# Kernel tuning notes

Measured on AMD Instinct MI355X. Metric: run time of the kernel, lower is better.

The kernel has to match this reference:

```python
import jax, jax.numpy as jnp
import numpy as np

B, S, D, L = 8, 512, 768, 200


def leaky(x, slope=0.2):
    return jnp.where(x >= 0, x, slope * x)


def l1_normalize(x, axis):
    # torch.nn.functional.normalize(p=1): x / max(sum|x|, 1e-12)
    return x / jnp.maximum(jnp.sum(jnp.abs(x), axis=axis, keepdims=True), 1e-12)


def setup_inputs() -> dict:
    key = jax.random.key(0)
    ks = jax.random.split(key, 16)
    s = 1.0 / np.sqrt(D)
    return {
        "doc_embedding": jax.random.normal(ks[0], (B, S, D), jnp.float32),
        "labels": jax.random.uniform(ks[1], (B, L), jnp.float32),
        "label_embed": jax.random.normal(ks[2], (L, D), jnp.float32),
        "label_adj": jax.random.uniform(ks[3], (L, L), jnp.float32),
        "w_gcn3": jax.random.uniform(ks[4], (D, D), jnp.float32, -s, s),
        "w_gcn5": jax.random.uniform(ks[5], (D, D), jnp.float32, -s, s),
        "w_ll1": jax.random.normal(ks[6], (D, D), jnp.float32) * s,
        "b_ll1": jax.random.normal(ks[7], (D,), jnp.float32) * s,
        "w_ll2": jax.random.normal(ks[8], (D, D), jnp.float32) * s,
        "b_ll2": jax.random.normal(ks[9], (D,), jnp.float32) * s,
        "w_lin": jax.random.normal(ks[10], (2 * D, D), jnp.float32) * (1.0 / np.sqrt(2 * D)),
        "b_lin": jax.random.normal(ks[11], (D,), jnp.float32) * s,
        "conv_w": jax.random.normal(ks[12], (L, 1, 9, 9), jnp.float32) * (1.0 / 9.0),
        "conv_b": jax.random.normal(ks[13], (L,), jnp.float32) * 0.01,
        "w_lin1": jax.random.normal(ks[14], (D, L), jnp.float32) * s,
        "b_lin1": jax.random.normal(ks[15], (L,), jnp.float32) * s,
    }


def reference(doc_embedding, labels, label_embed, label_adj, w_gcn3, w_gcn5,
              w_ll1, b_ll1, w_ll2, b_ll2, w_lin, b_lin, conv_w, conv_b,
              w_lin1, b_lin1):
    b = doc_embedding.shape[0]
    # stacked (replicated) label embeddings: [B, L, D]
    le = jnp.broadcast_to(label_embed, (b,) + label_embed.shape)

    # GCN3: adj @ (x @ W), leaky relu 0.2
    le = leaky(jnp.einsum('lm,bmd->bld', label_adj, le @ w_gcn3))

    # learned adjacency A = sigmoid(lin1(le) @ lin2(le)^T)   [B, L, L]
    q = le @ w_ll1 + b_ll1
    k = le @ w_ll2 + b_ll2
    A = jax.nn.sigmoid(jnp.einsum('bld,bmd->blm', q, k))

    # normalize_adj: D^{-1/2} with detached row sum; out = (A D)^T D
    row_sum = jax.lax.stop_gradient(jnp.sum(A, axis=1))  # [B, L]
    d_inv_sqrt = jnp.where(row_sum > 0, row_sum ** -0.5, 0.0)
    AD = A * d_inv_sqrt[:, None, :]                 # A @ diag(d)
    A_norm = jnp.swapaxes(AD, 1, 2) * d_inv_sqrt[:, None, :]

    # GCN5 with learned adj
    d_le = leaky(jnp.einsum('blm,bmd->bld', A_norm, le @ w_gcn5))

    le_cat = jnp.concatenate([le, d_le], axis=-1)   # [B, L, 2D]
    le_out = le_cat @ w_lin + b_lin                 # [B, L, D]

    le_out = l1_normalize(le_out, axis=-2)
    doc = l1_normalize(doc_embedding, axis=-2)

    # word-label attention map [B, S, L]
    wla = jnp.einsum('bsd,bld->bsl', doc, le_out)

    # conv2d 1 -> L channels, 9x9, pad 4 over [B, 1, S, L]
    att = jax.lax.conv_general_dilated(
        wla[:, None, :, :], conv_w, window_strides=(1, 1),
        padding=((4, 4), (4, 4)),
        dimension_numbers=('NCHW', 'OIHW', 'NCHW'))
    att = att + conv_b[None, :, None, None]         # [B, L, S, L]

    att = jnp.max(att, axis=1)                      # [B, S, L]
    att = jnp.max(att, axis=-1, keepdims=True)      # [B, S, 1]
    gate = jnp.tanh(att)

    h_enc = jnp.sum(gate * doc, axis=1)             # [B, D]
    label_output = jax.nn.sigmoid(h_enc @ w_lin1 + b_lin1)

    eps = 1e-7
    p = jnp.clip(label_output, eps, 1.0 - eps)
    loss = -jnp.mean(labels * jnp.log(p) + (1.0 - labels) * jnp.log(1.0 - p))
    return label_output, loss
```

## Files before the change

### kernel.cpp

```cpp
#include <hip/hip_runtime.h>
#include <hip/hip_bf16.h>
#include <math.h>

#define BB 8
#define SS 512
#define DD 768
#define LL 200

typedef __attribute__((ext_vector_type(8))) short bf16x8;
typedef __attribute__((ext_vector_type(4))) float f32x4;

__device__ inline short f2bf(float f) {
    unsigned u = __builtin_bit_cast(unsigned, f);
    unsigned r = (u + 0x7FFFu + ((u >> 16) & 1u)) >> 16;
    return (short)r;
}

#define LDP2 72

template<int EPI, bool TB>
__global__ __launch_bounds__(256) void mgemm_k(
    const short* __restrict__ A, int lda,
    const void* __restrict__ Bv, int ldb,
    const float* __restrict__ bias,
    const void* __restrict__ Bv2, const float* __restrict__ bias2, int nsplit,
    const void* __restrict__ Bv3, const float* __restrict__ bias3, int nsplit2,
    float* __restrict__ Cf, int ldc,
    short* __restrict__ Cb, int ldcb,
    short* __restrict__ Ct, int ldct, int nsplitT,
    int M, int N, int K)
{
    __shared__ __align__(16) short As[64 * LDP2];
    __shared__ __align__(16) short Bs[64 * LDP2];
    const int tid = threadIdx.x;
    const int bm = blockIdx.y * 64;
    const int bn = blockIdx.x * 64;
    int bnb = bn;
    if (!TB) {
        if (bn >= nsplit2)      { Bv = Bv3; bias = bias3; bnb = bn - nsplit2; }
        else if (bn >= nsplit)  { Bv = Bv2; bias = bias2; bnb = bn - nsplit; }
    }
    const int w = tid >> 6, lane = tid & 63, g = lane >> 4, ln = lane & 15;
    const int Kp = (K + 63) & ~63;
    const int nt = Kp >> 6;

    const int ar = tid >> 2, ac = tid & 3;
    const int bkk = tid >> 2, bc = tid & 3;

    f32x4 acc[4];
    #pragma unroll
    for (int i = 0; i < 4; ++i) acc[i] = (f32x4){0.f, 0.f, 0.f, 0.f};

    bf16x8 aR0 = {0,0,0,0,0,0,0,0}, aR1 = {0,0,0,0,0,0,0,0};
    bf16x8 bR0 = {0,0,0,0,0,0,0,0}, bR1 = {0,0,0,0,0,0,0,0};
    float  bF[16];
    #pragma unroll
    for (int j = 0; j < 16; ++j) bF[j] = 0.f;

    const int gmS = bm + ar;
    const bool aOk = (gmS < M);

    auto fetchA = [&](int k0) {
        if (aOk) {
            const short* p = A + (size_t)gmS * lda + k0 + ac * 16;
            aR0 = *(const bf16x8*)p;
            aR1 = *(const bf16x8*)(p + 8);
        }
    };
    auto fetchB = [&](int k0) {
        if (TB) {
            const short* Bt = (const short*)Bv;
            int gn = bn + ar;
            if (gn < N) {
                const short* p = Bt + (size_t)gn * ldb + k0 + ac * 16;
                bR0 = *(const bf16x8*)p;
                bR1 = *(const bf16x8*)(p + 8);
            }
        } else {
            const float* Bp = (const float*)Bv;
            int gk = k0 + bkk;
            int n0 = bnb + bc * 16;
            int gn0 = bn + bc * 16;
            if (gk < K) {
                const float* p = Bp + (size_t)gk * ldb + n0;
                if (gn0 + 16 <= N) {
                    #pragma unroll
                    for (int q = 0; q < 4; ++q) {
                        float4 x = *(const float4*)(p + q * 4);
                        bF[q*4+0]=x.x; bF[q*4+1]=x.y; bF[q*4+2]=x.z; bF[q*4+3]=x.w;
                    }
                } else {
                    #pragma unroll
                    for (int j = 0; j < 16; ++j) bF[j] = (gn0 + j < N) ? p[j] : 0.f;
                }
            } else {
                #pragma unroll
                for (int j = 0; j < 16; ++j) bF[j] = 0.f;
            }
        }
    };

    fetchA(0);
    fetchB(0);

    for (int t = 0; t < nt; ++t) {
        {
            short* pa = As + ar * LDP2 + ac * 16;
            *(bf16x8*)pa = aR0;
            *(bf16x8*)(pa + 8) = aR1;
        }
        if (TB) {
            short* pb = Bs + ar * LDP2 + ac * 16;
            *(bf16x8*)pb = bR0;
            *(bf16x8*)(pb + 8) = bR1;
        } else {
            #pragma unroll
            for (int j = 0; j < 16; ++j)
                Bs[(bc * 16 + j) * LDP2 + bkk] = f2bf(bF[j]);
        }
        __syncthreads();

        if (t + 1 < nt) {
            int k0 = (t + 1) << 6;
            fetchA(k0);
            fetchB(k0);
        }

        #pragma unroll
        for (int ks = 0; ks < 2; ++ks) {
            bf16x8 a = *(const bf16x8*)(As + (w * 16 + ln) * LDP2 + ks * 32 + g * 8);
            #pragma unroll
            for (int nb = 0; nb < 4; ++nb) {
                bf16x8 b = *(const bf16x8*)(Bs + (nb * 16 + ln) * LDP2 + ks * 32 + g * 8);
                acc[nb] = __builtin_amdgcn_mfma_f32_16x16x32_bf16(a, b, acc[nb], 0, 0, 0);
            }
        }
        __syncthreads();
    }

    #pragma unroll
    for (int nb = 0; nb < 4; ++nb) {
        int gn = bn + nb * 16 + ln;
        float bv = (bias && gn < N) ? bias[bnb + nb * 16 + ln] : 0.f;
        #pragma unroll
        for (int r = 0; r < 4; ++r) {
            int gm = bm + w * 16 + g * 4 + r;
            if (gm < M && gn < N) {
                float v = acc[nb][r] + bv;
                if (EPI == 1) v = (v >= 0.f) ? v : 0.2f * v;
                else if (EPI == 2) v = 1.f / (1.f + expf(-v));
                if (Cf) Cf[(size_t)gm * ldc + gn] = v;
                if (Cb) Cb[(size_t)gm * ldcb + gn] = f2bf(v);
                if (Ct && gn >= nsplitT)
                    Ct[(size_t)(gn - nsplitT) * ldct + gm] = f2bf(v);
            }
        }
    }
}

#define WP 168
#define TP 24
#define WTR 217
#define WROWS 208
#define APAD 256
#define BIGN (1 << 30)

__global__ void prep_k(const float* __restrict__ cw, const float* __restrict__ cb,
                       const float* __restrict__ adj,
                       short* __restrict__ wkg, short* __restrict__ adj_bf)
{
    int idx = blockIdx.x * blockDim.x + threadIdx.x;
    if (idx < WROWS * WP) {
        int o = idx / WP, kk = idx % WP;
        int kj = kk >> 4, ki = kk & 15;
        float v = 0.f;
        if (o < LL && kj < 9) {
            if (ki < 9) v = cw[o * 81 + ki * 9 + kj];
            else if (ki == 9 && kj == 0) v = cb[o];
        }
        wkg[idx] = f2bf(v);
        return;
    }
    idx -= WROWS * WP;
    if (idx < LL * APAD) {
        int r = idx / APAD, c = idx % APAD;
        adj_bf[idx] = f2bf(c < LL ? adj[r * LL + c] : 0.f);
    }
}

__global__ void ca_k(const float* __restrict__ A, short* __restrict__ An)
{
    int i = blockIdx.x;
    int j = threadIdx.x;
    float si = 0.f, sj = 0.f;
    for (int l = 0; l < LL; ++l) {
        si += A[l * LL + i];
        if (j < LL) sj += A[l * LL + j];
    }
    float di = (si > 0.f) ? (1.f / sqrtf(si)) : 0.f;
    float dj = (sj > 0.f) ? (1.f / sqrtf(sj)) : 0.f;
    float v = (j < LL) ? A[j * LL + i] * di * dj : 0.f;
    An[i * APAD + j] = f2bf(v);
}

__global__ void l1n_k(const float* __restrict__ X, short* __restrict__ Xb)
{
    int c = threadIdx.x >> 5, r = threadIdx.x & 31;
    int col = blockIdx.x * 8 + c;
    float s = 0.f;
    for (int l = r; l < LL; l += 32) s += fabsf(X[l * DD + col]);
    #pragma unroll
    for (int off = 16; off > 0; off >>= 1) s += __shfl_xor(s, off, 64);
    float inv = 1.f / fmaxf(s, 1e-12f);
    for (int l = r; l < LL; l += 32)
        Xb[l * DD + col] = f2bf(X[l * DD + col] * inv);
}

__global__ void docsum_k(const float* __restrict__ doc, float* __restrict__ denom)
{
    int dc = blockIdx.x, b = blockIdx.y;
    int dx = threadIdx.x & 63, sy = threadIdx.x >> 6;
    int d = dc * 64 + dx;
    float s = 0.f;
    for (int t = sy; t < SS; t += 4)
        s += fabsf(doc[((size_t)b * SS + t) * DD + d]);
    __shared__ float red[4][64];
    red[sy][dx] = s;
    __syncthreads();
    if (sy == 0)
        denom[b * DD + d] = fmaxf(red[0][dx] + red[1][dx] + red[2][dx] + red[3][dx], 1e-12f);
}

__global__ void docbf_k(const float* __restrict__ doc, const float* __restrict__ denom,
                        short* __restrict__ docb)
{
    int gid = blockIdx.x * blockDim.x + threadIdx.x;
    if (gid >= BB * SS * DD / 4) return;
    size_t base = (size_t)gid * 4;
    int d = (int)(base % DD);
    int b = (int)(base / ((size_t)SS * DD));
    float4 v = *(const float4*)(doc + base);
    float4 dn = *(const float4*)(denom + b * DD + d);
    short4 o;
    o.x = f2bf(v.x / dn.x);
    o.y = f2bf(v.y / dn.y);
    o.z = f2bf(v.z / dn.z);
    o.w = f2bf(v.w / dn.w);
    *(short4*)(docb + base) = o;
}

__global__ __launch_bounds__(512, 1) void conv_max_k(
    const float* __restrict__ wla,
    const short* __restrict__ wkg,
    float* __restrict__ gate)
{
    extern __shared__ short smem[];
    short* Wk   = smem;
    short* winT = Wk + WROWS * WP;
    short* wbf  = winT + 4 * WTR * TP;
    __shared__ float wredf[8];

    const int blk = blockIdx.x;
    const int b = blk >> 7;
    const int s0 = (blk & 127) << 2;
    const int tid = threadIdx.x;

    {
        const int4* src = (const int4*)wkg;
        int4* dst = (int4*)Wk;
        for (int i = tid; i < WROWS * WP / 8; i += 512) dst[i] = src[i];
    }
    for (int idx = tid; idx < 12 * 216; idx += 512) {
        int r = idx / 216, c = idx % 216;
        int sr = s0 - 4 + r, col = c - 4;
        float v = 0.f;
        if (sr >= 0 && sr < SS && col >= 0 && col < LL)
            v = wla[((size_t)b * SS + sr) * LL + col];
        wbf[idx] = f2bf(v);
    }
    __syncthreads();
    for (int idx = tid; idx < 4 * WTR; idx += 512) {
        int p = idx / WTR, r = idx % WTR;
        short vals[16];
        #pragma unroll
        for (int i = 0; i < 9; ++i) vals[i] = (r < 216) ? wbf[(p + i) * 216 + r] : (short)0;
        vals[9] = (short)0x3F80;
        #pragma unroll
        for (int i = 10; i < 16; ++i) vals[i] = 0;
        short* dstp = winT + (p * WTR + r) * TP;
        *(bf16x8*)dstp = *(const bf16x8*)vals;
        *(bf16x8*)(dstp + 8) = *(const bf16x8*)(vals + 8);
    }
    __syncthreads();

    const int w = tid >> 6;
    const int p = w >> 1;
    const int h = w & 1;
    const int lane = tid & 63;
    const int g = lane >> 4;
    const int ln = lane & 15;
    const short* WT = winT + p * WTR * TP;

    bf16x8 Af[7][5];
    #pragma unroll
    for (int s = 0; s < 7; ++s) {
        int st = h * 7 + s;
        if (st > 12) st = 12;
        #pragma unroll
        for (int j = 0; j < 5; ++j)
            Af[s][j] = *(const bf16x8*)(Wk + (st * 16 + ln) * WP + j * 32 + g * 8);
    }

    float lm = -INFINITY;

    auto loadB = [&](int nt, bf16x8 (&Bf)[5]) {
        #pragma unroll
        for (int j = 0; j < 5; ++j)
            Bf[j] = *(const bf16x8*)(WT + (nt * 16 + ln + 2 * j + (g >> 1)) * TP + (g & 1) * 8);
    };
    auto compute = [&](int nt, const bf16x8 (&Bf)[5]) {
        #pragma unroll
        for (int s = 0; s < 7; ++s) {
            if (h == 0 || s < 6) {
                int st = h * 7 + s;
                f32x4 acc = {0.f, 0.f, 0.f, 0.f};
                #pragma unroll
                for (int j = 0; j < 5; ++j)
                    acc = __builtin_amdgcn_mfma_f32_16x16x32_bf16(Af[s][j], Bf[j], acc, 0, 0, 0);
                float t = fmaxf(fmaxf(acc[0], acc[1]), fmaxf(acc[2], acc[3]));
                bool ok = (st < 12 || g < 2) && (nt < 12 || ln < 8);
                lm = ok ? fmaxf(lm, t) : lm;
            }
        }
    };

    bf16x8 B0[5], B1[5];
    loadB(0, B0);
    for (int nt = 0; nt < 12; nt += 2) {
        loadB(nt + 1, B1);
        compute(nt, B0);
        loadB(nt + 2, B0);
        compute(nt + 1, B1);
    }
    compute(12, B0);

    #pragma unroll
    for (int off = 32; off > 0; off >>= 1)
        lm = fmaxf(lm, __shfl_xor(lm, off, 64));
    if (lane == 0) wredf[w] = lm;
    __syncthreads();
    if (tid < 4)
        gate[((size_t)b << 9) + s0 + tid] = tanhf(fmaxf(wredf[2 * tid], wredf[2 * tid + 1]));
}

__global__ void henc_part_k(const float* __restrict__ doc, const float* __restrict__ gate,
                            float* __restrict__ hpart)
{
    int dc = blockIdx.x, sc = blockIdx.y, b = blockIdx.z;
    int dx = threadIdx.x & 63, sy = threadIdx.x >> 6;
    int d = dc * 64 + dx;
    float s = 0.f;
    for (int t = sy; t < 64; t += 4) {
        int srow = sc * 64 + t;
        s = fmaf(doc[((size_t)b * SS + srow) * DD + d], gate[b * SS + srow], s);
    }
    __shared__ float red[4][64];
    red[sy][dx] = s;
    __syncthreads();
    if (sy == 0)
        hpart[((size_t)b * 8 + sc) * DD + d] = red[0][dx] + red[1][dx] + red[2][dx] + red[3][dx];
}

__global__ void final2_k(const float* __restrict__ hpart, const float* __restrict__ denom,
                         const float* __restrict__ W, const float* __restrict__ bias,
                         float* __restrict__ out)
{
    int b = blockIdx.x, tid = threadIdx.x;
    __shared__ float hb[DD];
    for (int idx = tid; idx < DD; idx += 256) {
        float s = 0.f;
        #pragma unroll
        for (int sc = 0; sc < 8; ++sc) s += hpart[((size_t)b * 8 + sc) * DD + idx];
        hb[idx] = s / denom[b * DD + idx];
    }
    __syncthreads();
    int l = tid;
    if (l < LL) {
        float acc = bias[l];
        for (int d = 0; d < DD; ++d) acc = fmaf(hb[d], W[d * LL + l], acc);
        out[b * LL + l] = 1.f / (1.f + expf(-acc));
    }
}

__global__ void loss_k(const float* __restrict__ out, const float* __restrict__ labels,
                       float* __restrict__ loss_out)
{
    float s = 0.f;
    for (int i = threadIdx.x; i < BB * LL; i += 256) {
        float p = out[i];
        p = fminf(fmaxf(p, 1e-7f), 1.f - 1e-7f);
        float y = labels[i];
        s += y * logf(p) + (1.f - y) * logf(1.f - p);
    }
    #pragma unroll
    for (int off = 32; off > 0; off >>= 1) s += __shfl_down(s, off, 64);
    __shared__ float ws[4];
    if ((threadIdx.x & 63) == 0) ws[threadIdx.x >> 6] = s;
    __syncthreads();
    if (threadIdx.x == 0)
        loss_out[0] = -(ws[0] + ws[1] + ws[2] + ws[3]) / (float)(BB * LL);
}

static void mgemm(hipStream_t st, int epi, bool tb,
                  const short* A, int lda, const void* B, int ldb,
                  const float* bias,
                  const void* B2, const float* bias2, int nsplit,
                  const void* B3, const float* bias3, int nsplit2,
                  float* Cf, int ldc, short* Cb, int ldcb,
                  short* Ct, int ldct, int nsplitT,
                  int M, int N, int K)
{
    dim3 g((N + 63) / 64, (M + 63) / 64);
    if (!tb) {
        if (epi == 0)      mgemm_k<0, false><<<g, 256, 0, st>>>(A, lda, B, ldb, bias, B2, bias2, nsplit, B3, bias3, nsplit2, Cf, ldc, Cb, ldcb, Ct, ldct, nsplitT, M, N, K);
        else if (epi == 1) mgemm_k<1, false><<<g, 256, 0, st>>>(A, lda, B, ldb, bias, B2, bias2, nsplit, B3, bias3, nsplit2, Cf, ldc, Cb, ldcb, Ct, ldct, nsplitT, M, N, K);
        else               mgemm_k<2, false><<<g, 256, 0, st>>>(A, lda, B, ldb, bias, B2, bias2, nsplit, B3, bias3, nsplit2, Cf, ldc, Cb, ldcb, Ct, ldct, nsplitT, M, N, K);
    } else {
        if (epi == 0)      mgemm_k<0, true><<<g, 256, 0, st>>>(A, lda, B, ldb, bias, B2, bias2, nsplit, B3, bias3, nsplit2, Cf, ldc, Cb, ldcb, Ct, ldct, nsplitT, M, N, K);
        else if (epi == 1) mgemm_k<1, true><<<g, 256, 0, st>>>(A, lda, B, ldb, bias, B2, bias2, nsplit, B3, bias3, nsplit2, Cf, ldc, Cb, ldcb, Ct, ldct, nsplitT, M, N, K);
        else               mgemm_k<2, true><<<g, 256, 0, st>>>(A, lda, B, ldb, bias, B2, bias2, nsplit, B3, bias3, nsplit2, Cf, ldc, Cb, ldcb, Ct, ldct, nsplitT, M, N, K);
    }
}

extern "C" void kernel_launch(void* const* d_in, const int* in_sizes, int n_in,
                              void* d_out, int out_size, void* d_ws, size_t ws_size,
                              hipStream_t stream)
{
    const float* doc_emb   = (const float*)d_in[0];
    const float* labels    = (const float*)d_in[1];
    const float* label_emb = (const float*)d_in[2];
    const float* label_adj = (const float*)d_in[3];
    const float* w_gcn3    = (const float*)d_in[4];
    const float* w_gcn5    = (const float*)d_in[5];
    const float* w_ll1     = (const float*)d_in[6];
    const float* b_ll1     = (const float*)d_in[7];
    const float* w_ll2     = (const float*)d_in[8];
    const float* b_ll2     = (const float*)d_in[9];
    const float* w_lin     = (const float*)d_in[10];
    const float* b_lin     = (const float*)d_in[11];
    const float* conv_w    = (const float*)d_in[12];
    const float* conv_b    = (const float*)d_in[13];
    const float* w_lin1    = (const float*)d_in[14];
    const float* b_lin1    = (const float*)d_in[15];

    float* out = (float*)d_out;

    char* p = (char*)d_ws;
    auto alloc = [&](size_t bytes) { void* r = p; p += (bytes + 15) & ~(size_t)15; return r; };
    short* wkg       = (short*)alloc(WROWS * WP * 2);
    short* adj_bf    = (short*)alloc(200 * APAD * 2);
    short* E2_bf     = (short*)alloc(200 * 768 * 2);
    short* le_cat_bf = (short*)alloc(200 * 1536 * 2);
    short* qkh_bf    = (short*)alloc(200 * 2304 * 2);
    short* Ht        = (short*)alloc(768 * 256 * 2);
    float* Amat      = (float*)alloc(200 * 200 * 4);
    short* Anorm_bf  = (short*)alloc(200 * APAD * 2);
    float* le_out_f  = (float*)alloc(200 * 768 * 4);
    short* le_out_bf = (short*)alloc(200 * 768 * 2);
    float* denom     = (float*)alloc(BB * DD * 4);
    short* doc_nb    = (short*)alloc((size_t)BB * SS * DD * 2);
    float* wla       = (float*)alloc((size_t)BB * SS * LL * 4);
    float* gatev     = (float*)alloc(BB * SS * 4);
    float* hpart     = (float*)alloc(BB * 8 * DD * 4);

    prep_k<<<(WROWS * WP + LL * APAD + 255) / 256, 256, 0, stream>>>(
        conv_w, conv_b, label_adj, wkg, adj_bf);
    mgemm(stream, 0, false, adj_bf, APAD, label_emb, DD, nullptr,
          nullptr, nullptr, BIGN, nullptr, nullptr, BIGN,
          nullptr, 0, E2_bf, DD, nullptr, 0, BIGN, LL, DD, LL);
    mgemm(stream, 1, false, E2_bf, DD, w_gcn3, DD, nullptr,
          nullptr, nullptr, BIGN, nullptr, nullptr, BIGN,
          nullptr, 0, le_cat_bf, 1536, nullptr, 0, BIGN, LL, DD, DD);
    mgemm(stream, 0, false, le_cat_bf, 1536, w_ll1, DD, b_ll1,
          w_ll2, b_ll2, DD, w_gcn5, nullptr, 2 * DD,
          nullptr, 0, qkh_bf, 2304, Ht, 256, 2 * DD, LL, 3 * DD, DD);
    mgemm(stream, 2, true, qkh_bf, 2304, qkh_bf + DD, 2304, nullptr,
          nullptr, nullptr, BIGN, nullptr, nullptr, BIGN,
          Amat, LL, nullptr, 0, nullptr, 0, BIGN, LL, LL, DD);
    ca_k<<<LL, 256, 0, stream>>>(Amat, Anorm_bf);
    mgemm(stream, 1, true, Anorm_bf, APAD, Ht, 256, nullptr,
          nullptr, nullptr, BIGN, nullptr, nullptr, BIGN,
          nullptr, 0, le_cat_bf + DD, 1536, nullptr, 0, BIGN, LL, DD, LL);
    mgemm(stream, 0, false, le_cat_bf, 1536, w_lin, DD, b_lin,
          nullptr, nullptr, BIGN, nullptr, nullptr, BIGN,
          le_out_f, DD, nullptr, 0, nullptr, 0, BIGN, LL, DD, 2 * DD);
    l1n_k<<<96, 256, 0, stream>>>(le_out_f, le_out_bf);
    docsum_k<<<dim3(12, 8), 256, 0, stream>>>(doc_emb, denom);
    docbf_k<<<(BB * SS * DD / 4 + 255) / 256, 256, 0, stream>>>(doc_emb, denom, doc_nb);
    mgemm(stream, 0, true, doc_nb, DD, le_out_bf, DD, nullptr,
          nullptr, nullptr, BIGN, nullptr, nullptr, BIGN,
          wla, LL, nullptr, 0, nullptr, 0, BIGN, BB * SS, LL, DD);
    (void)hipFuncSetAttribute((const void*)conv_max_k,
                              hipFuncAttributeMaxDynamicSharedMemorySize, 116736);
    conv_max_k<<<1024, 512, 116736, stream>>>(wla, wkg, gatev);
    henc_part_k<<<dim3(12, 8, 8), 256, 0, stream>>>(doc_emb, gatev, hpart);
    final2_k<<<BB, 256, 0, stream>>>(hpart, denom, w_lin1, b_lin1, out);
    loss_k<<<1, 256, 0, stream>>>(out, labels, out + BB * LL);
}
```

Before: 298.3 us.

## Use 256-deep K tiles in GEMM and fuse doc normalization into prep

The GEMM kernel now stages 256-wide K tiles in dynamic shared memory instead of 64-wide tiles, which cuts the number of barriers and loop iterations for these small-M GEMMs. The non-transposed B loader reads one column per thread across 64 k rows, and the staging buffers grow to 64-entry arrays per thread, so register pressure goes up and occupancy is capped at one block. The doc L1-sum and bf16 conversion kernels are merged into the prep kernel. henc then reads the already-normalized bf16 doc instead of fp32 doc plus the denominator, which changes precision slightly.

```diff
diff --git a/kernel.cpp b/kernel.cpp
--- a/kernel.cpp
+++ b/kernel.cpp
@@ -15,11 +15,17 @@
     unsigned r = (u + 0x7FFFu + ((u >> 16) & 1u)) >> 16;
     return (short)r;
 }
-
-#define LDP2 72
+__device__ inline float bf2f(short s) {
+    unsigned u = ((unsigned)(unsigned short)s) << 16;
+    return __builtin_bit_cast(float, u);
+}
+
+#define LDP3 264
+#define BK3  256
+#define MGLDS (2 * 64 * LDP3 * 2)
 
 template<int EPI, bool TB>
-__global__ __launch_bounds__(256) void mgemm_k(
+__global__ __launch_bounds__(256, 1) void mgemm_k(
     const short* __restrict__ A, int lda,
     const void* __restrict__ Bv, int ldb,
     const float* __restrict__ bias,
@@ -30,8 +36,9 @@
     short* __restrict__ Ct, int ldct, int nsplitT,
     int M, int N, int K)
 {
-    __shared__ __align__(16) short As[64 * LDP2];
-    __shared__ __align__(16) short Bs[64 * LDP2];
+    extern __shared__ short dsm[];
+    short* As = dsm;
+    short* Bs = dsm + 64 * LDP3;
     const int tid = threadIdx.x;
     const int bm = blockIdx.y * 64;
     const int bn = blockIdx.x * 64;
@@ -41,30 +48,31 @@
         else if (bn >= nsplit)  { Bv = Bv2; bias = bias2; bnb = bn - nsplit; }
     }
     const int w = tid >> 6, lane = tid & 63, g = lane >> 4, ln = lane & 15;
-    const int Kp = (K + 63) & ~63;
-    const int nt = Kp >> 6;
+    const int Kp = (K + BK3 - 1) & ~(BK3 - 1);
+    const int nt = Kp >> 8;
 
     const int ar = tid >> 2, ac = tid & 3;
-    const int bkk = tid >> 2, bc = tid & 3;
+    const int bn_ = tid & 63, bko = (tid >> 6) * 64;
 
     f32x4 acc[4];
     #pragma unroll
     for (int i = 0; i < 4; ++i) acc[i] = (f32x4){0.f, 0.f, 0.f, 0.f};
 
-    bf16x8 aR0 = {0,0,0,0,0,0,0,0}, aR1 = {0,0,0,0,0,0,0,0};
-    bf16x8 bR0 = {0,0,0,0,0,0,0,0}, bR1 = {0,0,0,0,0,0,0,0};
-    float  bF[16];
-    #pragma unroll
-    for (int j = 0; j < 16; ++j) bF[j] = 0.f;
+    bf16x8 aR[8], bT[8];
+    #pragma unroll
+    for (int j = 0; j < 8; ++j) { aR[j] = (bf16x8){0,0,0,0,0,0,0,0}; bT[j] = (bf16x8){0,0,0,0,0,0,0,0}; }
+    float bF[64];
+    #pragma unroll
+    for (int j = 0; j < 64; ++j) bF[j] = 0.f;
 
     const int gmS = bm + ar;
     const bool aOk = (gmS < M);
 
     auto fetchA = [&](int k0) {
         if (aOk) {
-            const short* p = A + (size_t)gmS * lda + k0 + ac * 16;
-            aR0 = *(const bf16x8*)p;
-            aR1 = *(const bf16x8*)(p + 8);
+            const short* p = A + (size_t)gmS * lda + k0 + ac * 64;
+            #pragma unroll
+            for (int j = 0; j < 8; ++j) aR[j] = *(const bf16x8*)(p + j * 8);
         }
     };
     auto fetchB = [&](int k0) {
@@ -72,30 +80,16 @@
             const short* Bt = (const short*)Bv;
             int gn = bn + ar;
             if (gn < N) {
-                const short* p = Bt + (size_t)gn * ldb + k0 + ac * 16;
-                bR0 = *(const bf16x8*)p;
-                bR1 = *(const bf16x8*)(p + 8);
+                const short* p = Bt + (size_t)gn * ldb + k0 + ac * 64;
+                #pragma unroll
+                for (int j = 0; j < 8; ++j) bT[j] = *(const bf16x8*)(p + j * 8);
             }
         } else {
-            const float* Bp = (const float*)Bv;
-            int gk = k0 + bkk;
-            int n0 = bnb + bc * 16;
-            int gn0 = bn + bc * 16;
-            if (gk < K) {
-                const float* p = Bp + (size_t)gk * ldb + n0;
-                if (gn0 + 16 <= N) {
-                    #pragma unroll
-                    for (int q = 0; q < 4; ++q) {
-                        float4 x = *(const float4*)(p + q * 4);
-                        bF[q*4+0]=x.x; bF[q*4+1]=x.y; bF[q*4+2]=x.z; bF[q*4+3]=x.w;
-                    }
-                } else {
-                    #pragma unroll
-                    for (int j = 0; j < 16; ++j) bF[j] = (gn0 + j < N) ? p[j] : 0.f;
-                }
-            } else {
-                #pragma unroll
-                for (int j = 0; j < 16; ++j) bF[j] = 0.f;
+            const float* Bp = (const float*)Bv + (size_t)(bnb + bn_);
+            #pragma unroll
+            for (int j = 0; j < 64; ++j) {
+                int gk = k0 + bko + j;
+                bF[j] = (gk < K) ? Bp[(size_t)gk * ldb] : 0.f;
             }
         }
     };
@@ -105,33 +99,38 @@
 
     for (int t = 0; t < nt; ++t) {
         {
-            short* pa = As + ar * LDP2 + ac * 16;
-            *(bf16x8*)pa = aR0;
-            *(bf16x8*)(pa + 8) = aR1;
+            short* pa = As + ar * LDP3 + ac * 64;
+            #pragma unroll
+            for (int j = 0; j < 8; ++j) *(bf16x8*)(pa + j * 8) = aR[j];
         }
         if (TB) {
-            short* pb = Bs + ar * LDP2 + ac * 16;
-            *(bf16x8*)pb = bR0;
-            *(bf16x8*)(pb + 8) = bR1;
+            short* pb = Bs + ar * LDP3 + ac * 64;
+            #pragma unroll
+            for (int j = 0; j < 8; ++j) *(bf16x8*)(pb + j * 8) = bT[j];
         } else {
-            #pragma unroll
-            for (int j = 0; j < 16; ++j)
-                Bs[(bc * 16 + j) * LDP2 + bkk] = f2bf(bF[j]);
+            short* pb = Bs + bn_ * LDP3 + bko;
+            #pragma unroll
+            for (int q = 0; q < 8; ++q) {
+                bf16x8 v;
+                #pragma unroll
+                for (int e = 0; e < 8; ++e) v[e] = f2bf(bF[q * 8 + e]);
+                *(bf16x8*)(pb + q * 8) = v;
+            }
         }
         __syncthreads();
 
         if (t + 1 < nt) {
-            int k0 = (t + 1) << 6;
+            int k0 = (t + 1) << 8;
             fetchA(k0);
             fetchB(k0);
         }
 
         #pragma unroll
-        for (int ks = 0; ks < 2; ++ks) {
-            bf16x8 a = *(const bf16x8*)(As + (w * 16 + ln) * LDP2 + ks * 32 + g * 8);
+        for (int ks = 0; ks < 8; ++ks) {
+            bf16x8 a = *(const bf16x8*)(As + (w * 16 + ln) * LDP3 + ks * 32 + g * 8);
             #pragma unroll
             for (int nb = 0; nb < 4; ++nb) {
-                bf16x8 b = *(const bf16x8*)(Bs + (nb * 16 + ln) * LDP2 + ks * 32 + g * 8);
+                bf16x8 b = *(const bf16x8*)(Bs + (nb * 16 + ln) * LDP3 + ks * 32 + g * 8);
                 acc[nb] = __builtin_amdgcn_mfma_f32_16x16x32_bf16(a, b, acc[nb], 0, 0, 0);
             }
         }
@@ -165,11 +164,29 @@
 #define APAD 256
 #define BIGN (1 << 30)
 
-__global__ void prep_k(const float* __restrict__ cw, const float* __restrict__ cb,
-                       const float* __restrict__ adj,
-                       short* __restrict__ wkg, short* __restrict__ adj_bf)
-{
-    int idx = blockIdx.x * blockDim.x + threadIdx.x;
+__global__ void prep2_k(const float* __restrict__ cw, const float* __restrict__ cb,
+                        const float* __restrict__ adj, const float* __restrict__ doc,
+                        short* __restrict__ wkg, short* __restrict__ adj_bf,
+                        short* __restrict__ docb)
+{
+    if (blockIdx.x < 96) {
+        int u = blockIdx.x;
+        int dc = u % 12, b = u / 12;
+        int dx = threadIdx.x & 63, sy = threadIdx.x >> 6;
+        int d = dc * 64 + dx;
+        const float* pp = doc + (size_t)b * SS * DD + d;
+        float s = 0.f;
+        for (int t = sy; t < SS; t += 4) s += fabsf(pp[(size_t)t * DD]);
+        __shared__ float red[4][64];
+        red[sy][dx] = s;
+        __syncthreads();
+        float dn = fmaxf(red[0][dx] + red[1][dx] + red[2][dx] + red[3][dx], 1e-12f);
+        float inv = 1.f / dn;
+        short* qq = docb + (size_t)b * SS * DD + d;
+        for (int t = sy; t < SS; t += 4) qq[(size_t)t * DD] = f2bf(pp[(size_t)t * DD] * inv);
+        return;
+    }
+    int idx = (blockIdx.x - 96) * 256 + threadIdx.x;
     if (idx < WROWS * WP) {
         int o = idx / WP, kk = idx % WP;
         int kj = kk >> 4, ki = kk & 15;
@@ -214,39 +231,6 @@
     float inv = 1.f / fmaxf(s, 1e-12f);
     for (int l = r; l < LL; l += 32)
         Xb[l * DD + col] = f2bf(X[l * DD + col] * inv);
-}
-
-__global__ void docsum_k(const float* __restrict__ doc, float* __restrict__ denom)
-{
-    int dc = blockIdx.x, b = blockIdx.y;
-    int dx = threadIdx.x & 63, sy = threadIdx.x >> 6;
-    int d = dc * 64 + dx;
-    float s = 0.f;
-    for (int t = sy; t < SS; t += 4)
-        s += fabsf(doc[((size_t)b * SS + t) * DD + d]);
-    __shared__ float red[4][64];
-    red[sy][dx] = s;
-    __syncthreads();
-    if (sy == 0)
-        denom[b * DD + d] = fmaxf(red[0][dx] + red[1][dx] + red[2][dx] + red[3][dx], 1e-12f);
-}
-
-__global__ void docbf_k(const float* __restrict__ doc, const float* __restrict__ denom,
-                        short* __restrict__ docb)
-{
-    int gid = blockIdx.x * blockDim.x + threadIdx.x;
-    if (gid >= BB * SS * DD / 4) return;
-    size_t base = (size_t)gid * 4;
-    int d = (int)(base % DD);
-    int b = (int)(base / ((size_t)SS * DD));
-    float4 v = *(const float4*)(doc + base);
-    float4 dn = *(const float4*)(denom + b * DD + d);
-    short4 o;
-    o.x = f2bf(v.x / dn.x);
-    o.y = f2bf(v.y / dn.y);
-    o.z = f2bf(v.z / dn.z);
-    o.w = f2bf(v.w / dn.w);
-    *(short4*)(docb + base) = o;
 }
 
 __global__ __launch_bounds__(512, 1) void conv_max_k(
@@ -353,7 +337,7 @@
         gate[((size_t)b << 9) + s0 + tid] = tanhf(fmaxf(wredf[2 * tid], wredf[2 * tid + 1]));
 }
 
-__global__ void henc_part_k(const float* __restrict__ doc, const float* __restrict__ gate,
+__global__ void henc_part_k(const short* __restrict__ doc_nb, const float* __restrict__ gate,
                             float* __restrict__ hpart)
 {
     int dc = blockIdx.x, sc = blockIdx.y, b = blockIdx.z;
@@ -362,7 +346,7 @@
     float s = 0.f;
     for (int t = sy; t < 64; t += 4) {
         int srow = sc * 64 + t;
-        s = fmaf(doc[((size_t)b * SS + srow) * DD + d], gate[b * SS + srow], s);
+        s = fmaf(bf2f(doc_nb[((size_t)b * SS + srow) * DD + d]), gate[b * SS + srow], s);
     }
     __shared__ float red[4][64];
     red[sy][dx] = s;
@@ -371,7 +355,7 @@
         hpart[((size_t)b * 8 + sc) * DD + d] = red[0][dx] + red[1][dx] + red[2][dx] + red[3][dx];
 }
 
-__global__ void final2_k(const float* __restrict__ hpart, const float* __restrict__ denom,
+__global__ void final2_k(const float* __restrict__ hpart,
                          const float* __restrict__ W, const float* __restrict__ bias,
                          float* __restrict__ out)
 {
@@ -381,7 +365,7 @@
         float s = 0.f;
         #pragma unroll
         for (int sc = 0; sc < 8; ++sc) s += hpart[((size_t)b * 8 + sc) * DD + idx];
-        hb[idx] = s / denom[b * DD + idx];
+        hb[idx] = s;
     }
     __syncthreads();
     int l = tid;
@@ -421,15 +405,23 @@
                   int M, int N, int K)
 {
     dim3 g((N + 63) / 64, (M + 63) / 64);
+    #define LAUNCH(E, T) do { \
+        (void)hipFuncSetAttribute((const void*)mgemm_k<E, T>, \
+                                  hipFuncAttributeMaxDynamicSharedMemorySize, MGLDS); \
+        mgemm_k<E, T><<<g, 256, MGLDS, st>>>(A, lda, B, ldb, bias, B2, bias2, nsplit, \
+                                             B3, bias3, nsplit2, Cf, ldc, Cb, ldcb, \
+                                             Ct, ldct, nsplitT, M, N, K); \
+    } while (0)
     if (!tb) {
-        if (epi == 0)      mgemm_k<0, false><<<g, 256, 0, st>>>(A, lda, B, ldb, bias, B2, bias2, nsplit, B3, bias3, nsplit2, Cf, ldc, Cb, ldcb, Ct, ldct, nsplitT, M, N, K);
-        else if (epi == 1) mgemm_k<1, false><<<g, 256, 0, st>>>(A, lda, B, ldb, bias, B2, bias2, nsplit, B3, bias3, nsplit2, Cf, ldc, Cb, ldcb, Ct, ldct, nsplitT, M, N, K);
-        else               mgemm_k<2, false><<<g, 256, 0, st>>>(A, lda, B, ldb, bias, B2, bias2, nsplit, B3, bias3, nsplit2, Cf, ldc, Cb, ldcb, Ct, ldct, nsplitT, M, N, K);
+        if (epi == 0)      LAUNCH(0, false);
+        else if (epi == 1) LAUNCH(1, false);
+        else               LAUNCH(2, false);
     } else {
-        if (epi == 0)      mgemm_k<0, true><<<g, 256, 0, st>>>(A, lda, B, ldb, bias, B2, bias2, nsplit, B3, bias3, nsplit2, Cf, ldc, Cb, ldcb, Ct, ldct, nsplitT, M, N, K);
-        else if (epi == 1) mgemm_k<1, true><<<g, 256, 0, st>>>(A, lda, B, ldb, bias, B2, bias2, nsplit, B3, bias3, nsplit2, Cf, ldc, Cb, ldcb, Ct, ldct, nsplitT, M, N, K);
-        else               mgemm_k<2, true><<<g, 256, 0, st>>>(A, lda, B, ldb, bias, B2, bias2, nsplit, B3, bias3, nsplit2, Cf, ldc, Cb, ldcb, Ct, ldct, nsplitT, M, N, K);
-    }
+        if (epi == 0)      LAUNCH(0, true);
+        else if (epi == 1) LAUNCH(1, true);
+        else               LAUNCH(2, true);
+    }
+    #undef LAUNCH
 }
 
 extern "C" void kernel_launch(void* const* d_in, const int* in_sizes, int n_in,
@@ -467,14 +459,13 @@
     short* Anorm_bf  = (short*)alloc(200 * APAD * 2);
     float* le_out_f  = (float*)alloc(200 * 768 * 4);
     short* le_out_bf = (short*)alloc(200 * 768 * 2);
-    float* denom     = (float*)alloc(BB * DD * 4);
     short* doc_nb    = (short*)alloc((size_t)BB * SS * DD * 2);
     float* wla       = (float*)alloc((size_t)BB * SS * LL * 4);
     float* gatev     = (float*)alloc(BB * SS * 4);
     float* hpart     = (float*)alloc(BB * 8 * DD * 4);
 
-    prep_k<<<(WROWS * WP + LL * APAD + 255) / 256, 256, 0, stream>>>(
-        conv_w, conv_b, label_adj, wkg, adj_bf);
+    prep2_k<<<96 + (WROWS * WP + LL * APAD + 255) / 256, 256, 0, stream>>>(
+        conv_w, conv_b, label_adj, doc_emb, wkg, adj_bf, doc_nb);
     mgemm(stream, 0, false, adj_bf, APAD, label_emb, DD, nullptr,
           nullptr, nullptr, BIGN, nullptr, nullptr, BIGN,
           nullptr, 0, E2_bf, DD, nullptr, 0, BIGN, LL, DD, LL);
@@ -495,15 +486,13 @@
           nullptr, nullptr, BIGN, nullptr, nullptr, BIGN,
           le_out_f, DD, nullptr, 0, nullptr, 0, BIGN, LL, DD, 2 * DD);
     l1n_k<<<96, 256, 0, stream>>>(le_out_f, le_out_bf);
-    docsum_k<<<dim3(12, 8), 256, 0, stream>>>(doc_emb, denom);
-    docbf_k<<<(BB * SS * DD / 4 + 255) / 256, 256, 0, stream>>>(doc_emb, denom, doc_nb);
     mgemm(stream, 0, true, doc_nb, DD, le_out_bf, DD, nullptr,
           nullptr, nullptr, BIGN, nullptr, nullptr, BIGN,
           wla, LL, nullptr, 0, nullptr, 0, BIGN, BB * SS, LL, DD);
     (void)hipFuncSetAttribute((const void*)conv_max_k,
                               hipFuncAttributeMaxDynamicSharedMemorySize, 116736);
     conv_max_k<<<1024, 512, 116736, stream>>>(wla, wkg, gatev);
-    henc_part_k<<<dim3(12, 8, 8), 256, 0, stream>>>(doc_emb, gatev, hpart);
-    final2_k<<<BB, 256, 0, stream>>>(hpart, denom, w_lin1, b_lin1, out);
+    henc_part_k<<<dim3(12, 8, 8), 256, 0, stream>>>(doc_nb, gatev, hpart);
+    final2_k<<<BB, 256, 0, stream>>>(hpart, w_lin1, b_lin1, out);
     loss_k<<<1, 256, 0, stream>>>(out, labels, out + BB * LL);
 }
```

After: 306.7 us. 1.03x slower.
